# Performance work log

Hardware: AMD Instinct MI355X
Metric: run time of the kernel (lower is better)

Reference implementation:

```python
import jax, jax.numpy as jnp
import numpy as np

B, S, D, H = 4, 2048, 1024, 16
DK = D // H

def setup_inputs() -> dict:
    key = jax.random.key(0)
    ks = jax.random.split(key, 5)
    x = jax.random.normal(ks[0], (B, S, D), dtype=jnp.float32)
    scale = 1.0 / np.sqrt(D)
    Wq = jax.random.normal(ks[1], (D, D), dtype=jnp.float32) * scale
    Wk = jax.random.normal(ks[2], (D, D), dtype=jnp.float32) * scale
    Wv = jax.random.normal(ks[3], (D, D), dtype=jnp.float32) * scale
    Wo = jax.random.normal(ks[4], (D, D), dtype=jnp.float32) * scale
    return {"x": x, "Wq": Wq, "Wk": Wk, "Wv": Wv, "Wo": Wo}

def reference(x, Wq, Wk, Wv, Wo):
    # F.linear: y = x @ W.T  (weights stored torch-style [out, in])
    q = jnp.einsum('bsd,ed->bse', x, Wq).reshape(B, S, H, DK).transpose(0, 2, 1, 3)
    k = jnp.einsum('bsd,ed->bse', x, Wk).reshape(B, S, H, DK).transpose(0, 2, 1, 3)
    v = jnp.einsum('bsd,ed->bse', x, Wv).reshape(B, S, H, DK).transpose(0, 2, 1, 3)
    scores = jnp.einsum('bhqd,bhkd->bhqk', q, k) / jnp.sqrt(jnp.float32(DK))
    attn = jax.nn.softmax(scores, axis=-1)  # dropout p=0.0 -> identity
    out = jnp.einsum('bhqk,bhkd->bhqd', attn, v)
    out = out.transpose(0, 2, 1, 3).reshape(B, S, D)
    return jnp.einsum('bsd,ed->bse', out, Wo)
```

## Files before the change

### kernel.cpp

```cpp
#include <hip/hip_runtime.h>
#include <hip/hip_bf16.h>

#define B_ 4
#define S_ 2048
#define D_ 1024
#define H_ 16
#define DK_ 64

typedef __attribute__((ext_vector_type(8))) short short8;
typedef __attribute__((ext_vector_type(4))) float floatx4;
typedef __attribute__((ext_vector_type(16))) float floatx16;
typedef __attribute__((ext_vector_type(4))) unsigned int uint4v;

#define QSCL 0.1803368801111204f

static __device__ __forceinline__ unsigned short f2bf(float f) {
    unsigned int u = __float_as_uint(f);
    u += 0x7fffu + ((u >> 16) & 1u);
    return (unsigned short)(u >> 16);
}

static __device__ __forceinline__ unsigned int pack2bf_trunc(float a, float b) {
    return __builtin_amdgcn_perm(__float_as_uint(b), __float_as_uint(a), 0x07060302u);
}

static __device__ __forceinline__ unsigned int pack2bf(float a, float b) {
    return (unsigned int)f2bf(a) | ((unsigned int)f2bf(b) << 16);
}

#define PLSWAP(a, b) asm volatile("v_permlane32_swap_b32 %0, %1" : "+v"(a), "+v"(b))

struct CastAll {
    const float* x;
    const float* w[4];
    unsigned short* xd;
    unsigned short* wd[4];
};

__global__ void cast_all_kernel(CastAll a) {
    int i = blockIdx.x * blockDim.x + threadIdx.x;
    const float* s;
    unsigned short* d;
    int j;
    if (i < 2097152) {
        s = a.x; d = a.xd; j = i;
    } else {
        int k = i - 2097152;
        int w = k >> 18;
        j = k & 262143;
        s = a.w[w]; d = a.wd[w];
    }
    float4 v = ((const float4*)s)[j];
    ushort4 o;
    o.x = f2bf(v.x); o.y = f2bf(v.y); o.z = f2bf(v.z); o.w = f2bf(v.w);
    ((ushort4*)d)[j] = o;
}

template <typename OutT, bool VT2>
__global__ __launch_bounds__(256) void gemm_bt(
    const unsigned short* __restrict__ A,
    const unsigned short* __restrict__ W0,
    const unsigned short* __restrict__ W1,
    const unsigned short* __restrict__ W2,
    OutT* __restrict__ C0, OutT* __restrict__ C1, OutT* __restrict__ C2,
    int M, int N, int K)
{
    __shared__ __align__(16) unsigned short At[128 * 64];
    __shared__ __align__(16) unsigned short Bt[128 * 64];

    const unsigned short* W = (blockIdx.z == 0) ? W0 : ((blockIdx.z == 1) ? W1 : W2);
    OutT* C = (blockIdx.z == 0) ? C0 : ((blockIdx.z == 1) ? C1 : C2);

    const int n0 = blockIdx.x * 128;
    const int m0 = blockIdx.y * 128;
    const int wv = threadIdx.x >> 6;
    const int ln = threadIdx.x & 63;
    const int l31 = ln & 31;
    const int half = ln >> 5;
    const int wm = (wv >> 1) * 64;
    const int wn = (wv & 1) * 64;

    floatx16 acc[2][2];
#pragma unroll
    for (int mt = 0; mt < 2; mt++)
#pragma unroll
        for (int nt = 0; nt < 2; nt++)
#pragma unroll
            for (int e = 0; e < 16; e++) acc[mt][nt][e] = 0.f;

    const int lr = ln >> 3;
    const int lc = (((ln & 7) ^ lr) * 8);
    const int sw = (l31 & 7);

    for (int k0 = 0; k0 < K; k0 += 64) {
        __syncthreads();
#pragma unroll
        for (int c = 0; c < 4; c++) {
            int rowA = wv * 32 + c * 8;
            const unsigned short* gA = A + (size_t)(m0 + rowA + lr) * K + k0 + lc;
            __builtin_amdgcn_global_load_lds(
                (const __attribute__((address_space(1))) void*)gA,
                (__attribute__((address_space(3))) void*)&At[rowA * 64], 16, 0, 0);
            const unsigned short* gB = W + (size_t)(n0 + rowA + lr) * K + k0 + lc;
            __builtin_amdgcn_global_load_lds(
                (const __attribute__((address_space(1))) void*)gB,
                (__attribute__((address_space(3))) void*)&Bt[rowA * 64], 16, 0, 0);
        }
        __syncthreads();

#pragma unroll
        for (int ks = 0; ks < 4; ks++) {
            const int slot = ((ks * 2 + half) ^ sw) * 8;
            short8 af[2], bf[2];
#pragma unroll
            for (int mt = 0; mt < 2; mt++)
                af[mt] = *(const short8*)&At[(wm + mt * 32 + l31) * 64 + slot];
#pragma unroll
            for (int nt = 0; nt < 2; nt++)
                bf[nt] = *(const short8*)&Bt[(wn + nt * 32 + l31) * 64 + slot];
#pragma unroll
            for (int mt = 0; mt < 2; mt++)
#pragma unroll
                for (int nt = 0; nt < 2; nt++)
                    acc[mt][nt] = __builtin_amdgcn_mfma_f32_32x32x16_bf16(af[mt], bf[nt], acc[mt][nt], 0, 0, 0);
        }
    }

    const float esc = (VT2 && blockIdx.z == 0) ? QSCL : 1.0f;

    if constexpr (VT2) {
        if (blockIdx.z == 2) {
            unsigned short* Vt = (unsigned short*)C;
#pragma unroll
            for (int mt = 0; mt < 2; mt++)
#pragma unroll
                for (int nt = 0; nt < 2; nt++)
#pragma unroll
                    for (int rg = 0; rg < 4; rg++) {
                        int col = n0 + wn + nt * 32 + l31;
                        int row0 = m0 + wm + mt * 32 + 4 * half + 8 * rg;
                        int bb = row0 >> 11, ss = row0 & 2047;
                        size_t addr = ((size_t)(bb * 1024 + col)) * 2048 + ss;
                        uint2 pk;
                        pk.x = pack2bf(acc[mt][nt][4 * rg + 0], acc[mt][nt][4 * rg + 1]);
                        pk.y = pack2bf(acc[mt][nt][4 * rg + 2], acc[mt][nt][4 * rg + 3]);
                        *(uint2*)(Vt + addr) = pk;
                    }
            return;
        }
    }

#pragma unroll
    for (int mt = 0; mt < 2; mt++)
#pragma unroll
        for (int nt = 0; nt < 2; nt++)
#pragma unroll
            for (int rg = 0; rg < 4; rg++)
#pragma unroll
                for (int r = 0; r < 4; r++) {
                    int row = m0 + wm + mt * 32 + 4 * half + 8 * rg + r;
                    int col = n0 + wn + nt * 32 + l31;
                    float v = acc[mt][nt][4 * rg + r] * esc;
                    if constexpr (sizeof(OutT) == 2)
                        C[(size_t)row * N + col] = (OutT)f2bf(v);
                    else
                        C[(size_t)row * N + col] = v;
                }
}

__global__ __launch_bounds__(256, 4) void flash_attn(
    const unsigned short* __restrict__ Q,
    const unsigned short* __restrict__ K,
    const unsigned short* __restrict__ Vt,
    unsigned short* __restrict__ O)
{
    __shared__ __align__(16) unsigned short Kt[64 * 64];
    __shared__ __align__(16) unsigned short VT[64 * 64];

    const int qt = blockIdx.x;
    const int h = blockIdx.y;
    const int b = blockIdx.z;
    const int tid = threadIdx.x;
    const int wv = tid >> 6;
    const int ln = tid & 63;
    const int l31 = ln & 31;
    const int half = ln >> 5;

    const size_t base = ((size_t)b * S_) * D_ + (size_t)h * DK_;
    const size_t vtbase = ((size_t)(b * 1024 + h * 64)) * (size_t)S_;

    const int qrow = qt * 128 + wv * 32 + l31;
    short8 qf[4];
    {
        const unsigned short* qp = Q + base + (size_t)qrow * D_ + half * 8;
#pragma unroll
        for (int ks = 0; ks < 4; ks++) qf[ks] = *(const short8*)(qp + ks * 16);
    }

    short8 ones;
#pragma unroll
    for (int e = 0; e < 8; e++) ones[e] = (short)0x3F80;

    floatx16 Oacc[2], lacc;
#pragma unroll
    for (int mt = 0; mt < 2; mt++)
#pragma unroll
        for (int e = 0; e < 16; e++) Oacc[mt][e] = 0.f;
#pragma unroll
    for (int e = 0; e < 16; e++) lacc[e] = 0.f;

    const int lrow = ln >> 3;
    const int lchk = (ln & 7) ^ lrow;
    const unsigned short* kg = K + base + (size_t)(wv * 16 + lrow) * D_ + lchk * 8;
    const unsigned short* vg = Vt + vtbase + (size_t)(wv * 16 + lrow) * S_ + lchk * 8;
    unsigned short* ldsK0 = &Kt[(wv * 16) * 64];
    unsigned short* ldsK1 = &Kt[(wv * 16 + 8) * 64];
    unsigned short* ldsV0 = &VT[(wv * 16) * 64];
    unsigned short* ldsV1 = &VT[(wv * 16 + 8) * 64];

    const int sw = (l31 & 7);

    for (int kt = 0; kt < S_ / 64; kt++) {
        __syncthreads();
        __builtin_amdgcn_global_load_lds(
            (const __attribute__((address_space(1))) void*)kg,
            (__attribute__((address_space(3))) void*)ldsK0, 16, 0, 0);
        __builtin_amdgcn_global_load_lds(
            (const __attribute__((address_space(1))) void*)(kg + 8 * D_),
            (__attribute__((address_space(3))) void*)ldsK1, 16, 0, 0);
        __builtin_amdgcn_global_load_lds(
            (const __attribute__((address_space(1))) void*)vg,
            (__attribute__((address_space(3))) void*)ldsV0, 16, 0, 0);
        __builtin_amdgcn_global_load_lds(
            (const __attribute__((address_space(1))) void*)(vg + 8 * S_),
            (__attribute__((address_space(3))) void*)ldsV1, 16, 0, 0);
        kg += (size_t)64 * D_;
        vg += 64;
        __syncthreads();

        floatx16 sac[2];
#pragma unroll
        for (int mt = 0; mt < 2; mt++) {
#pragma unroll
            for (int e = 0; e < 16; e++) sac[mt][e] = 0.f;
#pragma unroll
            for (int ks = 0; ks < 4; ks++) {
                const int slot = ((ks * 2 + half) ^ sw) * 8;
                short8 kf = *(const short8*)&Kt[(mt * 32 + l31) * 64 + slot];
                sac[mt] = __builtin_amdgcn_mfma_f32_32x32x16_bf16(kf, qf[ks], sac[mt], 0, 0, 0);
            }
        }

        uint2 run[2][4];
#pragma unroll
        for (int mt = 0; mt < 2; mt++)
#pragma unroll
            for (int g = 0; g < 4; g++) {
                float p0 = __builtin_amdgcn_exp2f(sac[mt][4 * g + 0]);
                float p1 = __builtin_amdgcn_exp2f(sac[mt][4 * g + 1]);
                float p2 = __builtin_amdgcn_exp2f(sac[mt][4 * g + 2]);
                float p3 = __builtin_amdgcn_exp2f(sac[mt][4 * g + 3]);
                run[mt][g].x = pack2bf_trunc(p0, p1);
                run[mt][g].y = pack2bf_trunc(p2, p3);
            }

#pragma unroll
        for (int mt = 0; mt < 2; mt++)
#pragma unroll
            for (int t = 0; t < 2; t++) {
                PLSWAP(run[mt][2 * t].x, run[mt][2 * t + 1].x);
                PLSWAP(run[mt][2 * t].y, run[mt][2 * t + 1].y);
            }

#pragma unroll
        for (int mt2 = 0; mt2 < 2; mt2++)
#pragma unroll
            for (int t = 0; t < 2; t++) {
                int ks = mt2 * 2 + t;
                uint4v u = {run[mt2][2 * t].x, run[mt2][2 * t].y,
                            run[mt2][2 * t + 1].x, run[mt2][2 * t + 1].y};
                short8 pf = __builtin_bit_cast(short8, u);
                const int slot = ((ks * 2 + half) ^ sw) * 8;
#pragma unroll
                for (int mt = 0; mt < 2; mt++) {
                    short8 vf = *(const short8*)&VT[(mt * 32 + l31) * 64 + slot];
                    Oacc[mt] = __builtin_amdgcn_mfma_f32_32x32x16_bf16(vf, pf, Oacc[mt], 0, 0, 0);
                }
                lacc = __builtin_amdgcn_mfma_f32_32x32x16_bf16(ones, pf, lacc, 0, 0, 0);
            }
    }

    float inv = 1.0f / lacc[0];

#pragma unroll
    for (int mt = 0; mt < 2; mt++)
#pragma unroll
        for (int g = 0; g < 4; g++) {
            uint2 pk;
            pk.x = pack2bf(Oacc[mt][4 * g + 0] * inv, Oacc[mt][4 * g + 1] * inv);
            pk.y = pack2bf(Oacc[mt][4 * g + 2] * inv, Oacc[mt][4 * g + 3] * inv);
            *(uint2*)(O + base + (size_t)qrow * D_ + mt * 32 + 8 * g + 4 * half) = pk;
        }
}

extern "C" void kernel_launch(void* const* d_in, const int* in_sizes, int n_in,
                              void* d_out, int out_size, void* d_ws, size_t ws_size,
                              hipStream_t stream) {
    const float* x  = (const float*)d_in[0];
    const float* Wq = (const float*)d_in[1];
    const float* Wk = (const float*)d_in[2];
    const float* Wv = (const float*)d_in[3];
    const float* Wo = (const float*)d_in[4];
    float* out = (float*)d_out;

    char* ws = (char*)d_ws;
    const size_t MB = 1024 * 1024;
    unsigned short* xb  = (unsigned short*)(ws);
    unsigned short* wqb = (unsigned short*)(ws + 16 * MB);
    unsigned short* wkb = (unsigned short*)(ws + 18 * MB);
    unsigned short* wvb = (unsigned short*)(ws + 20 * MB);
    unsigned short* wob = (unsigned short*)(ws + 22 * MB);
    unsigned short* Qb  = (unsigned short*)(ws + 24 * MB);
    unsigned short* Kb  = (unsigned short*)(ws + 40 * MB);
    unsigned short* Vtb = (unsigned short*)(ws + 56 * MB);
    unsigned short* Ob  = (unsigned short*)(ws);

    CastAll ca;
    ca.x = x; ca.xd = xb;
    ca.w[0] = Wq; ca.w[1] = Wk; ca.w[2] = Wv; ca.w[3] = Wo;
    ca.wd[0] = wqb; ca.wd[1] = wkb; ca.wd[2] = wvb; ca.wd[3] = wob;
    cast_all_kernel<<<12288, 256, 0, stream>>>(ca);

    dim3 gq(D_ / 128, (B_ * S_) / 128, 3);
    gemm_bt<unsigned short, true><<<gq, 256, 0, stream>>>(
        xb, wqb, wkb, wvb, Qb, Kb, Vtb, B_ * S_, D_, D_);

    dim3 gf(S_ / 128, H_, B_);
    flash_attn<<<gf, 256, 0, stream>>>(Qb, Kb, Vtb, Ob);

    dim3 go(D_ / 128, (B_ * S_) / 128, 1);
    gemm_bt<float, false><<<go, 256, 0, stream>>>(
        Ob, wob, wob, wob, out, out, out, B_ * S_, D_, D_);
}
```

Before: 291.5 us.

## Double-buffer K/V tiles in LDS and compute softmax row sums with scalar adds

Flash attention now keeps two LDS buffers for K and V. The next tile's global-to-LDS loads are issued right after the barrier, so they overlap the MFMA and exp work on the current tile, and the second barrier per iteration is gone. The row sum, which an extra MFMA against a ones vector used to produce, is now built by adding the fp32 exponentials per lane and combining the two half-waves with one xor-shuffle. The cost is double the LDS per block. Using unrounded fp32 values for the denominator changes numerics slightly.

```diff
diff --git a/kernel.cpp b/kernel.cpp
--- a/kernel.cpp
+++ b/kernel.cpp
@@ -174,8 +174,8 @@
     const unsigned short* __restrict__ Vt,
     unsigned short* __restrict__ O)
 {
-    __shared__ __align__(16) unsigned short Kt[64 * 64];
-    __shared__ __align__(16) unsigned short VT[64 * 64];
+    __shared__ __align__(16) unsigned short Kt[2][64 * 64];
+    __shared__ __align__(16) unsigned short VT[2][64 * 64];
 
     const int qt = blockIdx.x;
     const int h = blockIdx.y;
@@ -197,46 +197,58 @@
         for (int ks = 0; ks < 4; ks++) qf[ks] = *(const short8*)(qp + ks * 16);
     }
 
-    short8 ones;
-#pragma unroll
-    for (int e = 0; e < 8; e++) ones[e] = (short)0x3F80;
-
-    floatx16 Oacc[2], lacc;
+    floatx16 Oacc[2];
 #pragma unroll
     for (int mt = 0; mt < 2; mt++)
 #pragma unroll
         for (int e = 0; e < 16; e++) Oacc[mt][e] = 0.f;
-#pragma unroll
-    for (int e = 0; e < 16; e++) lacc[e] = 0.f;
+    float l_i = 0.f;
 
     const int lrow = ln >> 3;
     const int lchk = (ln & 7) ^ lrow;
     const unsigned short* kg = K + base + (size_t)(wv * 16 + lrow) * D_ + lchk * 8;
     const unsigned short* vg = Vt + vtbase + (size_t)(wv * 16 + lrow) * S_ + lchk * 8;
-    unsigned short* ldsK0 = &Kt[(wv * 16) * 64];
-    unsigned short* ldsK1 = &Kt[(wv * 16 + 8) * 64];
-    unsigned short* ldsV0 = &VT[(wv * 16) * 64];
-    unsigned short* ldsV1 = &VT[(wv * 16 + 8) * 64];
+    const int ldsRow0 = (wv * 16) * 64;
+    const int ldsRow1 = (wv * 16 + 8) * 64;
 
     const int sw = (l31 & 7);
-
-    for (int kt = 0; kt < S_ / 64; kt++) {
+    const int NT = S_ / 64;
+
+    __builtin_amdgcn_global_load_lds(
+        (const __attribute__((address_space(1))) void*)kg,
+        (__attribute__((address_space(3))) void*)&Kt[0][ldsRow0], 16, 0, 0);
+    __builtin_amdgcn_global_load_lds(
+        (const __attribute__((address_space(1))) void*)(kg + 8 * D_),
+        (__attribute__((address_space(3))) void*)&Kt[0][ldsRow1], 16, 0, 0);
+    __builtin_amdgcn_global_load_lds(
+        (const __attribute__((address_space(1))) void*)vg,
+        (__attribute__((address_space(3))) void*)&VT[0][ldsRow0], 16, 0, 0);
+    __builtin_amdgcn_global_load_lds(
+        (const __attribute__((address_space(1))) void*)(vg + 8 * S_),
+        (__attribute__((address_space(3))) void*)&VT[0][ldsRow1], 16, 0, 0);
+    kg += (size_t)64 * D_;
+    vg += 64;
+
+    for (int kt = 0; kt < NT; kt++) {
+        const int cur = kt & 1;
         __syncthreads();
-        __builtin_amdgcn_global_load_lds(
-            (const __attribute__((address_space(1))) void*)kg,
-            (__attribute__((address_space(3))) void*)ldsK0, 16, 0, 0);
-        __builtin_amdgcn_global_load_lds(
-            (const __attribute__((address_space(1))) void*)(kg + 8 * D_),
-            (__attribute__((address_space(3))) void*)ldsK1, 16, 0, 0);
-        __builtin_amdgcn_global_load_lds(
-            (const __attribute__((address_space(1))) void*)vg,
-            (__attribute__((address_space(3))) void*)ldsV0, 16, 0, 0);
-        __builtin_amdgcn_global_load_lds(
-            (const __attribute__((address_space(1))) void*)(vg + 8 * S_),
-            (__attribute__((address_space(3))) void*)ldsV1, 16, 0, 0);
-        kg += (size_t)64 * D_;
-        vg += 64;
-        __syncthreads();
+
+        if (kt + 1 < NT) {
+            __builtin_amdgcn_global_load_lds(
+                (const __attribute__((address_space(1))) void*)kg,
+                (__attribute__((address_space(3))) void*)&Kt[cur ^ 1][ldsRow0], 16, 0, 0);
+            __builtin_amdgcn_global_load_lds(
+                (const __attribute__((address_space(1))) void*)(kg + 8 * D_),
+                (__attribute__((address_space(3))) void*)&Kt[cur ^ 1][ldsRow1], 16, 0, 0);
+            __builtin_amdgcn_global_load_lds(
+                (const __attribute__((address_space(1))) void*)vg,
+                (__attribute__((address_space(3))) void*)&VT[cur ^ 1][ldsRow0], 16, 0, 0);
+            __builtin_amdgcn_global_load_lds(
+                (const __attribute__((address_space(1))) void*)(vg + 8 * S_),
+                (__attribute__((address_space(3))) void*)&VT[cur ^ 1][ldsRow1], 16, 0, 0);
+            kg += (size_t)64 * D_;
+            vg += 64;
+        }
 
         floatx16 sac[2];
 #pragma unroll
@@ -246,7 +258,7 @@
 #pragma unroll
             for (int ks = 0; ks < 4; ks++) {
                 const int slot = ((ks * 2 + half) ^ sw) * 8;
-                short8 kf = *(const short8*)&Kt[(mt * 32 + l31) * 64 + slot];
+                short8 kf = *(const short8*)&Kt[cur][(mt * 32 + l31) * 64 + slot];
                 sac[mt] = __builtin_amdgcn_mfma_f32_32x32x16_bf16(kf, qf[ks], sac[mt], 0, 0, 0);
             }
         }
@@ -260,6 +272,7 @@
                 float p1 = __builtin_amdgcn_exp2f(sac[mt][4 * g + 1]);
                 float p2 = __builtin_amdgcn_exp2f(sac[mt][4 * g + 2]);
                 float p3 = __builtin_amdgcn_exp2f(sac[mt][4 * g + 3]);
+                l_i += (p0 + p1) + (p2 + p3);
                 run[mt][g].x = pack2bf_trunc(p0, p1);
                 run[mt][g].y = pack2bf_trunc(p2, p3);
             }
@@ -283,14 +296,14 @@
                 const int slot = ((ks * 2 + half) ^ sw) * 8;
 #pragma unroll
                 for (int mt = 0; mt < 2; mt++) {
-                    short8 vf = *(const short8*)&VT[(mt * 32 + l31) * 64 + slot];
+                    short8 vf = *(const short8*)&VT[cur][(mt * 32 + l31) * 64 + slot];
                     Oacc[mt] = __builtin_amdgcn_mfma_f32_32x32x16_bf16(vf, pf, Oacc[mt], 0, 0, 0);
                 }
-                lacc = __builtin_amdgcn_mfma_f32_32x32x16_bf16(ones, pf, lacc, 0, 0, 0);
             }
     }
 
-    float inv = 1.0f / lacc[0];
+    l_i += __shfl_xor(l_i, 32);
+    float inv = 1.0f / l_i;
 
 #pragma unroll
     for (int mt = 0; mt < 2; mt++)
```

After: 286.0 us. Within noise of the previous version (-1.9%).
